# Kernel optimization log

Hardware: AMD Instinct MI355X
Metric: run time of the kernel (lower is better)

## Reference

```python
import jax, jax.numpy as jnp
import numpy as np
from jax import lax

W_WIN = 7  # window size from init_kwargs


def _dwconv(x, k):
    """Depthwise 2D conv, SAME padding, kernel k: [C,1,kh,kw] (OIHW)."""
    C = x.shape[1]
    p = k.shape[-1] // 2
    return lax.conv_general_dilated(
        x, k, window_strides=(1, 1), padding=[(p, p), (p, p)],
        feature_group_count=C, dimension_numbers=("NCHW", "OIHW", "NCHW"))


def setup_inputs() -> dict:
    key = jax.random.key(0)
    ks = jax.random.split(key, 6)
    B, C, H, Wd = 1, 48, 56, 56
    x = jax.random.normal(ks[0], (B, C, H, Wd), dtype=jnp.float32)
    # small init scale keeps the softmax logits (dot/49) in a sane range
    w3 = jax.random.normal(ks[1], (C, 1, 3, 3), dtype=jnp.float32) * 0.1
    w5 = jax.random.normal(ks[2], (C, 1, 5, 5), dtype=jnp.float32) * 0.1
    w7 = jax.random.normal(ks[3], (C, 1, 7, 7), dtype=jnp.float32) * 0.1
    pw = jax.random.normal(ks[4], (C, 3 * C, 1, 1), dtype=jnp.float32) * 0.05
    pb = jax.random.normal(ks[5], (C,), dtype=jnp.float32) * 0.01
    return {"x": x, "w3": w3, "w5": w5, "w7": w7, "pw": pw, "pb": pb}


def reference(x, w3, w5, w7, pw, pb):
    B, C, H, Wd = x.shape
    w = W_WIN
    # multi-scale depthwise branch, concat on channels -> [B, 3C, H, W]
    y = jnp.concatenate([_dwconv(x, w3), _dwconv(x, w5), _dwconv(x, w7)], axis=1)
    pad_h = (-H) % w
    pad_w = (-Wd) % w
    if pad_h or pad_w:  # static Python ints -> jit-safe
        y = jnp.pad(y, ((0, 0), (0, 0), (0, pad_h), (0, pad_w)), mode="reflect")
    Hp, Wp = y.shape[2], y.shape[3]
    nH, nW = Hp // w, Wp // w
    C3 = 3 * C
    # equivalent to torch unfold(2,w,w).unfold(3,w,w).permute(0,1,2,4,3,5)
    # .reshape(B,3C,nH*nW,w*w): same row-major linearization
    yw = y.reshape(B, C3, nH * nW, w * w)
    # rows: (B, nH*nW, 3C) flattened -> N x (w*w)
    yf = yw.transpose(0, 2, 1, 3).reshape(B * nH * nW * C3, w * w)
    # full N x N self-attention over all rows (faithful to the original)
    attn = jax.nn.softmax((yf @ yf.T) / (w * w), axis=-1)
    y_hat = (attn @ yf).reshape(B, nH, nW, C3, w, w)
    y_hat = y_hat.transpose(0, 3, 1, 4, 2, 5).reshape(B, C3, nH * w, nW * w)
    y_hat = y_hat[:, :, :H, :Wd]
    # 1x1 projection 3C -> C, plus residual
    out = jnp.einsum("oi,bihw->bohw", pw[:, :, 0, 0], y_hat) + pb[None, :, None, None]
    return x + out
```

## Files before the change

### kernel.cpp

```cpp
#include <hip/hip_runtime.h>

typedef unsigned int uint;
typedef unsigned short ushort;
typedef __attribute__((ext_vector_type(8))) short bf16x8;
typedef __attribute__((ext_vector_type(4))) float f32x4;

#define C_IN   48
#define C3     144
#define HW     56
#define SSP    3136
#define DW     49
#define DPAD   64
#define NROWS  9216

#define NSPLIT 8
#define TPS    18

#define CSC 0.02944245f

#define YF_B    0
#define YFT_B   1179648
#define OPART_B 2359296
#define ESUM_B  (OPART_B + 8 * DW * NROWS * 2)

__device__ __forceinline__ ushort f32_to_bf16_rne(float x) {
  uint b = __float_as_uint(x);
  b += 0x7fffu + ((b >> 16) & 1u);
  return (ushort)(b >> 16);
}
__device__ __forceinline__ float bf16_to_f32(ushort u) {
  return __uint_as_float(((uint)u) << 16);
}
__device__ __forceinline__ void async_copy16(const void* g, void* l) {
  __builtin_amdgcn_global_load_lds(
      (const __attribute__((address_space(1))) unsigned int*)g,
      (__attribute__((address_space(3))) unsigned int*)l, 16, 0, 0);
}

__global__ __launch_bounds__(256) void conv_kernel(
    const float* __restrict__ x, const float* __restrict__ w3,
    const float* __restrict__ w5, const float* __restrict__ w7,
    ushort* __restrict__ yf) {
  int idx = blockIdx.x * 256 + threadIdx.x;
  int r = idx >> 6, t = idx & 63;
  ushort outv = 0;
  if (t < DW) {
    int g = r / C3, c3 = r - g * C3;
    int flat = g * DW + t;
    int h = flat / HW, w = flat - h * HW;
    int grp = c3 / C_IN, c = c3 - grp * C_IN;
    const float* wk; int ks;
    if (grp == 0)      { wk = w3 + c * 9;  ks = 3; }
    else if (grp == 1) { wk = w5 + c * 25; ks = 5; }
    else               { wk = w7 + c * 49; ks = 7; }
    int p = ks >> 1;
    const float* xc = x + c * SSP;
    float val = 0.f;
    for (int dy = 0; dy < ks; dy++) {
      int hy = h + dy - p;
      if (hy < 0 || hy >= HW) continue;
      const float* xr = xc + hy * HW;
      const float* wr = wk + dy * ks;
      for (int dx = 0; dx < ks; dx++) {
        int wx = w + dx - p;
        if (wx < 0 || wx >= HW) continue;
        val += xr[wx] * wr[dx];
      }
    }
    outv = f32_to_bf16_rne(val);
  }
  yf[idx] = outv;
}

__global__ __launch_bounds__(256) void transpose_kernel(
    const ushort* __restrict__ yf, ushort* __restrict__ yfT) {
  __shared__ ushort tile[64][72];
  int r0 = blockIdx.x * 64;
  int tid = threadIdx.x;
  int rr = tid >> 2, cb = (tid & 3) * 16;
  *(bf16x8*)&tile[rr][cb]     = *(const bf16x8*)&yf[(r0 + rr) * 64 + cb];
  *(bf16x8*)&tile[rr][cb + 8] = *(const bf16x8*)&yf[(r0 + rr) * 64 + cb + 8];
  __syncthreads();
  int t = tid >> 2, rb = (tid & 3) * 16;
  ushort tmp[16];
#pragma unroll
  for (int i = 0; i < 16; i++) tmp[i] = tile[rb + i][t];
  if (t == 56) {
#pragma unroll
    for (int i = 0; i < 16; i++) tmp[i] = 0x3F80;
  }
  *(bf16x8*)&yfT[t * NROWS + r0 + rb]     = *(bf16x8*)&tmp[0];
  *(bf16x8*)&yfT[t * NROWS + r0 + rb + 8] = *(bf16x8*)&tmp[8];
}

__global__ __launch_bounds__(256, 3) void attn_kernel(
    const ushort* __restrict__ yf, const ushort* __restrict__ yfT,
    ushort* __restrict__ opart, float* __restrict__ esum_g) {
  __shared__ __align__(16) char smem[51200];

  const int tid = threadIdx.x;
  const int w = tid >> 6, lane = tid & 63;
  const int q = lane >> 4, c = lane & 15;
  const int m0 = blockIdx.x * 128 + w * 32;
  const int sp = blockIdx.y;
  ushort* Pm = (ushort*)(smem + 32768) + w * (32 * 72);

  bf16x8 qf[2][2];
#pragma unroll
  for (int mt = 0; mt < 2; mt++)
#pragma unroll
    for (int ds = 0; ds < 2; ds++) {
      bf16x8 raw = *(const bf16x8*)&yf[(m0 + mt * 16 + c) * 64 + ds * 32 + q * 8];
      short tmp[8];
#pragma unroll
      for (int j = 0; j < 8; j++)
        tmp[j] = (short)f32_to_bf16_rne(bf16_to_f32((ushort)raw[j]) * CSC);
      qf[mt][ds] = *(bf16x8*)tmp;
    }

  f32x4 o[4][2];
#pragma unroll
  for (int dt = 0; dt < 4; dt++)
#pragma unroll
    for (int mt = 0; mt < 2; mt++) o[dt][mt] = (f32x4)0.f;

  const int s0 = w, s1 = w + 4;

  {
    const int k0 = (sp * TPS) * 64;
    char* Kb = smem;
    char* Vb = smem + 16384;
    async_copy16(yf + (k0 + lane) * 64 + s0 * 8, Kb + s0 * 1024);
    async_copy16(yf + (k0 + lane) * 64 + s1 * 8, Kb + s1 * 1024);
    async_copy16(yfT + lane * NROWS + k0 + s0 * 8, Vb + s0 * 1024);
    async_copy16(yfT + lane * NROWS + k0 + s1 * 8, Vb + s1 * 1024);
  }
  __syncthreads();

  for (int it = 0; it < TPS; it++) {
    const int cur = it & 1;
    if (it + 1 < TPS) {
      const int k1 = (sp * TPS + it + 1) * 64;
      char* Kb = smem + (cur ^ 1) * 8192;
      char* Vb = smem + 16384 + (cur ^ 1) * 8192;
      async_copy16(yf + (k1 + lane) * 64 + s0 * 8, Kb + s0 * 1024);
      async_copy16(yf + (k1 + lane) * 64 + s1 * 8, Kb + s1 * 1024);
      async_copy16(yfT + lane * NROWS + k1 + s0 * 8, Vb + s0 * 1024);
      async_copy16(yfT + lane * NROWS + k1 + s1 * 8, Vb + s1 * 1024);
    }

    const char* Kb = smem + cur * 8192;
    const char* Vb = smem + 16384 + cur * 8192;

    f32x4 s[4][2];
#pragma unroll
    for (int nt = 0; nt < 4; nt++) {
      bf16x8 a0 = *(const bf16x8*)(Kb + q * 1024 + (nt * 16 + c) * 16);
      bf16x8 a1 = *(const bf16x8*)(Kb + (4 + q) * 1024 + (nt * 16 + c) * 16);
      s[nt][0] = (f32x4)0.f; s[nt][1] = (f32x4)0.f;
      s[nt][0] = __builtin_amdgcn_mfma_f32_16x16x32_bf16(a0, qf[0][0], s[nt][0], 0, 0, 0);
      s[nt][1] = __builtin_amdgcn_mfma_f32_16x16x32_bf16(a0, qf[1][0], s[nt][1], 0, 0, 0);
      s[nt][0] = __builtin_amdgcn_mfma_f32_16x16x32_bf16(a1, qf[0][1], s[nt][0], 0, 0, 0);
      s[nt][1] = __builtin_amdgcn_mfma_f32_16x16x32_bf16(a1, qf[1][1], s[nt][1], 0, 0, 0);
    }

#pragma unroll
    for (int nt = 0; nt < 4; nt++)
#pragma unroll
      for (int mt = 0; mt < 2; mt++) {
        f32x4 sv = s[nt][mt];
        float p0 = __builtin_amdgcn_exp2f(sv[0]);
        float p1 = __builtin_amdgcn_exp2f(sv[1]);
        float p2 = __builtin_amdgcn_exp2f(sv[2]);
        float p3 = __builtin_amdgcn_exp2f(sv[3]);
        uint d0 = (__float_as_uint(p0) >> 16) | (__float_as_uint(p1) & 0xffff0000u);
        uint d1 = (__float_as_uint(p2) >> 16) | (__float_as_uint(p3) & 0xffff0000u);
        *(uint2*)&Pm[(mt * 16 + c) * 72 + nt * 16 + q * 4] = make_uint2(d0, d1);
      }

    bf16x8 bp[2][2];
#pragma unroll
    for (int mt = 0; mt < 2; mt++)
#pragma unroll
      for (int nc = 0; nc < 2; nc++)
        bp[mt][nc] = *(const bf16x8*)&Pm[(mt * 16 + c) * 72 + nc * 32 + q * 8];
#pragma unroll
    for (int dt = 0; dt < 4; dt++) {
      bf16x8 v0 = *(const bf16x8*)(Vb + q * 1024 + (dt * 16 + c) * 16);
      bf16x8 v1 = *(const bf16x8*)(Vb + (4 + q) * 1024 + (dt * 16 + c) * 16);
      o[dt][0] = __builtin_amdgcn_mfma_f32_16x16x32_bf16(v0, bp[0][0], o[dt][0], 0, 0, 0);
      o[dt][1] = __builtin_amdgcn_mfma_f32_16x16x32_bf16(v0, bp[1][0], o[dt][1], 0, 0, 0);
      o[dt][0] = __builtin_amdgcn_mfma_f32_16x16x32_bf16(v1, bp[0][1], o[dt][0], 0, 0, 0);
      o[dt][1] = __builtin_amdgcn_mfma_f32_16x16x32_bf16(v1, bp[1][1], o[dt][1], 0, 0, 0);
    }

    __syncthreads();
  }

#pragma unroll
  for (int dt = 0; dt < 4; dt++)
#pragma unroll
    for (int mt = 0; mt < 2; mt++)
#pragma unroll
      for (int r = 0; r < 4; r++) {
        int d = dt * 16 + q * 4 + r;
        int m = m0 + mt * 16 + c;
        float v = o[dt][mt][r];
        if (d < DW) {
          opart[(sp * DW + d) * NROWS + m] = f32_to_bf16_rne(v);
        } else if (d == 56) {
          esum_g[sp * NROWS + m] = v;
        }
      }
}

__global__ __launch_bounds__(256) void fuse_pw_kernel(
    const ushort* __restrict__ opart, const float* __restrict__ esum_g,
    const float* __restrict__ x, const float* __restrict__ pw,
    const float* __restrict__ pb, float* __restrict__ out) {
  __shared__ float vb[13 * 145];
  __shared__ float inv_es[144];
  const int g = blockIdx.x, tch = blockIdx.y;
  const int t0 = tch * 13;
  const int t1 = (t0 + 13 < DW) ? t0 + 13 : DW;
  const int nt = t1 - t0;
  const int tid = threadIdx.x;

  if (tid < 144) {
    int r = g * C3 + tid;
    float e = 0.f;
#pragma unroll
    for (int sp = 0; sp < NSPLIT; sp++) e += esum_g[sp * NROWS + r];
    inv_es[tid] = 1.f / e;
  }
  __syncthreads();

  for (int j = tid; j < nt * 144; j += 256) {
    int tt = j / 144, i = j - tt * 144;
    int r = g * C3 + i, t = t0 + tt;
    float ov = 0.f;
#pragma unroll
    for (int sp = 0; sp < NSPLIT; sp++)
      ov += bf16_to_f32(opart[(sp * DW + t) * NROWS + r]);
    vb[tt * 145 + i] = ov * inv_es[i];
  }
  __syncthreads();

  for (int j = tid; j < C_IN * nt; j += 256) {
    int o = j / nt, tt = j - o * nt;
    int t = t0 + tt;
    const float* pwo = pw + o * C3;
    const float* vrow = &vb[tt * 145];
    float a0 = 0.f, a1 = 0.f, a2 = 0.f, a3 = 0.f;
#pragma unroll
    for (int i = 0; i < C3; i += 4) {
      float4 wv = *(const float4*)&pwo[i];
      a0 += wv.x * vrow[i];
      a1 += wv.y * vrow[i + 1];
      a2 += wv.z * vrow[i + 2];
      a3 += wv.w * vrow[i + 3];
    }
    float acc = (a0 + a1) + (a2 + a3);
    int nh = g >> 3, nw = g & 7;
    int th = t / 7, tw = t - th * 7;
    int oidx = o * SSP + (nh * 7 + th) * HW + (nw * 7 + tw);
    out[oidx] = x[oidx] + pb[o] + acc;
  }
}

extern "C" void kernel_launch(void* const* d_in, const int* in_sizes, int n_in,
                              void* d_out, int out_size, void* d_ws, size_t ws_size,
                              hipStream_t stream) {
  const float* x  = (const float*)d_in[0];
  const float* w3 = (const float*)d_in[1];
  const float* w5 = (const float*)d_in[2];
  const float* w7 = (const float*)d_in[3];
  const float* pw = (const float*)d_in[4];
  const float* pb = (const float*)d_in[5];
  float* out = (float*)d_out;
  char* ws = (char*)d_ws;

  ushort* yf    = (ushort*)(ws + YF_B);
  ushort* yfT   = (ushort*)(ws + YFT_B);
  ushort* opart = (ushort*)(ws + OPART_B);
  float*  esum  = (float*)(ws + ESUM_B);

  conv_kernel<<<(NROWS * DPAD) / 256, 256, 0, stream>>>(x, w3, w5, w7, yf);
  transpose_kernel<<<NROWS / 64, 256, 0, stream>>>(yf, yfT);
  attn_kernel<<<dim3(NROWS / 128, NSPLIT), 256, 0, stream>>>(yf, yfT, opart, esum);
  fuse_pw_kernel<<<dim3(64, 4), 256, 0, stream>>>(opart, esum, x, pw, pb, out);
}
```

Measured before the change: 126.8 us.

## Fuse conv with transpose kernel and double attention key split count

```diff
diff --git a/kernel.cpp b/kernel.cpp
--- a/kernel.cpp
+++ b/kernel.cpp
@@ -13,15 +13,15 @@
 #define DPAD   64
 #define NROWS  9216
 
-#define NSPLIT 8
-#define TPS    18
+#define NSPLIT 16
+#define TPS    9
 
 #define CSC 0.02944245f
 
 #define YF_B    0
 #define YFT_B   1179648
 #define OPART_B 2359296
-#define ESUM_B  (OPART_B + 8 * DW * NROWS * 2)
+#define ESUM_B  (OPART_B + NSPLIT * DW * NROWS * 2)
 
 __device__ __forceinline__ ushort f32_to_bf16_rne(float x) {
   uint b = __float_as_uint(x);
@@ -37,60 +37,65 @@
       (__attribute__((address_space(3))) unsigned int*)l, 16, 0, 0);
 }
 
-__global__ __launch_bounds__(256) void conv_kernel(
+__global__ __launch_bounds__(256) void conv_t_kernel(
     const float* __restrict__ x, const float* __restrict__ w3,
     const float* __restrict__ w5, const float* __restrict__ w7,
-    ushort* __restrict__ yf) {
-  int idx = blockIdx.x * 256 + threadIdx.x;
-  int r = idx >> 6, t = idx & 63;
-  ushort outv = 0;
-  if (t < DW) {
-    int g = r / C3, c3 = r - g * C3;
-    int flat = g * DW + t;
-    int h = flat / HW, w = flat - h * HW;
-    int grp = c3 / C_IN, c = c3 - grp * C_IN;
-    const float* wk; int ks;
-    if (grp == 0)      { wk = w3 + c * 9;  ks = 3; }
-    else if (grp == 1) { wk = w5 + c * 25; ks = 5; }
-    else               { wk = w7 + c * 49; ks = 7; }
-    int p = ks >> 1;
-    const float* xc = x + c * SSP;
-    float val = 0.f;
-    for (int dy = 0; dy < ks; dy++) {
-      int hy = h + dy - p;
-      if (hy < 0 || hy >= HW) continue;
-      const float* xr = xc + hy * HW;
-      const float* wr = wk + dy * ks;
-      for (int dx = 0; dx < ks; dx++) {
-        int wx = w + dx - p;
-        if (wx < 0 || wx >= HW) continue;
-        val += xr[wx] * wr[dx];
+    ushort* __restrict__ yf, ushort* __restrict__ yfT) {
+  __shared__ ushort tile[64][72];
+  const int tid = threadIdx.x;
+  const int r0 = blockIdx.x * 64;
+  const int rr = tid >> 2, qc = tid & 3;
+  const int r = r0 + rr;
+  const int g = r / C3, c3 = r - g * C3;
+  const int grp = c3 / C_IN, c = c3 - grp * C_IN;
+  const float* wk; int ks;
+  if (grp == 0)      { wk = w3 + c * 9;  ks = 3; }
+  else if (grp == 1) { wk = w5 + c * 25; ks = 5; }
+  else               { wk = w7 + c * 49; ks = 7; }
+  const int p = ks >> 1;
+  const float* xc = x + c * SSP;
+  const int tbase = qc * 16;
+
+  ushort vals[16];
+#pragma unroll
+  for (int i = 0; i < 16; i++) {
+    int t = tbase + i;
+    ushort ov = 0;
+    if (t < DW) {
+      int flat = g * DW + t;
+      int h = flat / HW, w = flat - h * HW;
+      float val = 0.f;
+      for (int dy = 0; dy < ks; dy++) {
+        int hy = h + dy - p;
+        if (hy < 0 || hy >= HW) continue;
+        const float* xr = xc + hy * HW;
+        const float* wr = wk + dy * ks;
+        for (int dx = 0; dx < ks; dx++) {
+          int wx = w + dx - p;
+          if (wx < 0 || wx >= HW) continue;
+          val += xr[wx] * wr[dx];
+        }
       }
-    }
-    outv = f32_to_bf16_rne(val);
-  }
-  yf[idx] = outv;
-}
-
-__global__ __launch_bounds__(256) void transpose_kernel(
-    const ushort* __restrict__ yf, ushort* __restrict__ yfT) {
-  __shared__ ushort tile[64][72];
-  int r0 = blockIdx.x * 64;
-  int tid = threadIdx.x;
-  int rr = tid >> 2, cb = (tid & 3) * 16;
-  *(bf16x8*)&tile[rr][cb]     = *(const bf16x8*)&yf[(r0 + rr) * 64 + cb];
-  *(bf16x8*)&tile[rr][cb + 8] = *(const bf16x8*)&yf[(r0 + rr) * 64 + cb + 8];
-  __syncthreads();
-  int t = tid >> 2, rb = (tid & 3) * 16;
+      ov = f32_to_bf16_rne(val);
+    }
+    vals[i] = ov;
+  }
+  *(bf16x8*)&yf[r * 64 + tbase]     = *(bf16x8*)&vals[0];
+  *(bf16x8*)&yf[r * 64 + tbase + 8] = *(bf16x8*)&vals[8];
+  *(bf16x8*)&tile[rr][tbase]        = *(bf16x8*)&vals[0];
+  *(bf16x8*)&tile[rr][tbase + 8]    = *(bf16x8*)&vals[8];
+  __syncthreads();
+
+  const int d = tid >> 2, rb = (tid & 3) * 16;
   ushort tmp[16];
 #pragma unroll
-  for (int i = 0; i < 16; i++) tmp[i] = tile[rb + i][t];
-  if (t == 56) {
+  for (int i = 0; i < 16; i++) tmp[i] = tile[rb + i][d];
+  if (d == 56) {
 #pragma unroll
     for (int i = 0; i < 16; i++) tmp[i] = 0x3F80;
   }
-  *(bf16x8*)&yfT[t * NROWS + r0 + rb]     = *(bf16x8*)&tmp[0];
-  *(bf16x8*)&yfT[t * NROWS + r0 + rb + 8] = *(bf16x8*)&tmp[8];
+  *(bf16x8*)&yfT[d * NROWS + r0 + rb]     = *(bf16x8*)&tmp[0];
+  *(bf16x8*)&yfT[d * NROWS + r0 + rb + 8] = *(bf16x8*)&tmp[8];
 }
 
 __global__ __launch_bounds__(256, 3) void attn_kernel(
@@ -194,7 +199,7 @@
       o[dt][1] = __builtin_amdgcn_mfma_f32_16x16x32_bf16(v1, bp[1][1], o[dt][1], 0, 0, 0);
     }
 
-    __syncthreads();
+    if (it + 1 < TPS) __syncthreads();
   }
 
 #pragma unroll
@@ -285,8 +290,7 @@
   ushort* opart = (ushort*)(ws + OPART_B);
   float*  esum  = (float*)(ws + ESUM_B);
 
-  conv_kernel<<<(NROWS * DPAD) / 256, 256, 0, stream>>>(x, w3, w5, w7, yf);
-  transpose_kernel<<<NROWS / 64, 256, 0, stream>>>(yf, yfT);
+  conv_t_kernel<<<NROWS / 64, 256, 0, stream>>>(x, w3, w5, w7, yf, yfT);
   attn_kernel<<<dim3(NROWS / 128, NSPLIT), 256, 0, stream>>>(yf, yfT, opart, esum);
   fuse_pw_kernel<<<dim3(64, 4), 256, 0, stream>>>(opart, esum, x, pw, pb, out);
 }
```

New measurement: 238.2 us. 1.88x slower.
